# Kernel tuning notes

Hardware: AMD Instinct MI355X
Metric: run time of the kernel (lower is better)

## Reference

```python
import jax, jax.numpy as jnp
import numpy as np

DIM = 1024
HID = 256
MAXT = 2048
B = 4
T = 2048


def setup_inputs() -> dict:
    key = jax.random.key(0)
    ks = jax.random.split(key, 10)
    s_in = 1.0 / np.sqrt(DIM)   # keeps K ~ N(0,1) so exp(K) is stable
    s_h = 1.0 / np.sqrt(HID)
    # xavier-uniform bound for square wbias: sqrt(6/(T+T))
    wb_bound = float(np.sqrt(6.0 / (MAXT + MAXT)))
    return {
        "x": jax.random.normal(ks[0], (B, T, DIM), dtype=jnp.float32),
        "Wq": jax.random.normal(ks[1], (DIM, HID), dtype=jnp.float32) * s_in,
        "bq": jnp.zeros((HID,), dtype=jnp.float32),
        "Wk": jax.random.normal(ks[2], (DIM, HID), dtype=jnp.float32) * s_in,
        "bk": jnp.zeros((HID,), dtype=jnp.float32),
        "Wv": jax.random.normal(ks[3], (DIM, HID), dtype=jnp.float32) * s_in,
        "bv": jnp.zeros((HID,), dtype=jnp.float32),
        "Wp": jax.random.normal(ks[4], (HID, DIM), dtype=jnp.float32) * s_h,
        "bp": jnp.zeros((DIM,), dtype=jnp.float32),
        "wbias": jax.random.uniform(ks[5], (MAXT, MAXT), dtype=jnp.float32,
                                    minval=-wb_bound, maxval=wb_bound),
    }


def reference(x, Wq, bq, Wk, bk, Wv, bv, Wp, bp, wbias):
    Bn, Tn, _ = x.shape
    Q = x @ Wq + bq            # [B,T,H]
    K = x @ Wk + bk            # [B,T,H]
    V = x @ Wv + bv            # [B,T,H]
    ew = jnp.exp(wbias[:Tn, :Tn])          # [T,T]
    eK = jnp.exp(K)                         # [B,T,H]
    num = jnp.einsum('ts,bsh->bth', ew, eK * V)   # [B,T,H]
    den = jnp.einsum('ts,bsh->bth', ew, eK)       # [B,T,H]
    Yt = jax.nn.sigmoid(Q) * (num / den)          # [B,T,H]
    return Yt @ Wp + bp                            # [B,T,DIM]
```

## Files before the change

### kernel.cpp

```cpp
#include <hip/hip_runtime.h>
#include <hip/hip_bf16.h>


typedef __attribute__((ext_vector_type(8))) short bf16x8;
typedef __attribute__((ext_vector_type(4))) float f32x4;

static __device__ __forceinline__ unsigned short f2b(float f) {
  __hip_bfloat16 h = __float2bfloat16(f);
  return __builtin_bit_cast(unsigned short, h);
}

static __device__ __forceinline__ void gld16(const void* g, const void* l) {
  __builtin_amdgcn_global_load_lds((const __attribute__((address_space(1))) void*)g,
                                   (__attribute__((address_space(3))) void*)l, 16, 0, 0);
}

static __device__ __forceinline__ void core128(
    const unsigned short* __restrict__ A_blk,
    const unsigned short* __restrict__ Bt_blk,
    long sA, long sB, int nk, char* AsB, char* BsB, f32x4 acc[4][4],
    int tid, int wr, int wc, int fr, int fkb)
{
  const int srow = tid >> 2;
  const int sk   = (tid & 3) * 8;
  const unsigned short* ap0 = A_blk + (long)srow * sA + sk;
  const unsigned short* ap1 = ap0 + 64 * sA;
  const unsigned short* bp0 = Bt_blk + (long)srow * sB + sk;
  const unsigned short* bp1 = bp0 + 64 * sB;
  char* la0 = AsB + tid * 16;
  char* la1 = AsB + 4096 + tid * 16;
  char* lb0 = BsB + tid * 16;
  char* lb1 = BsB + 4096 + tid * 16;

  for (int kt = 0; kt < nk; ++kt) {
    gld16(ap0, la0);
    gld16(ap1, la1);
    gld16(bp0, lb0);
    gld16(bp1, lb1);
    ap0 += 32; ap1 += 32; bp0 += 32; bp1 += 32;
    asm volatile("s_waitcnt vmcnt(0)" ::: "memory");
    __syncthreads();

    bf16x8 av[4], bv[4];
#pragma unroll
    for (int m = 0; m < 4; ++m)
      av[m] = *(const bf16x8*)(AsB + (wr * 64 + m * 16 + fr) * 64 + fkb);
#pragma unroll
    for (int n = 0; n < 4; ++n)
      bv[n] = *(const bf16x8*)(BsB + (wc * 64 + n * 16 + fr) * 64 + fkb);
#pragma unroll
    for (int m = 0; m < 4; ++m)
#pragma unroll
      for (int n = 0; n < 4; ++n)
        acc[m][n] = __builtin_amdgcn_mfma_f32_16x16x32_bf16(av[m], bv[n], acc[m][n], 0, 0, 0);
    __syncthreads();
  }
}

__global__ __launch_bounds__(256) void gemm_bt(
    const unsigned short* __restrict__ A, const unsigned short* __restrict__ Bt,
    float* __restrict__ C, const float* __restrict__ bias,
    int M, int N, int K, int Ksub)
{
  __shared__ char AsB[8192];
  __shared__ char BsB[8192];
  const int tid = threadIdx.x, lane = tid & 63, wave = tid >> 6;
  const int wr = wave >> 1, wc = wave & 1;
  const int fr = lane & 15, fkb = (lane >> 4) * 16, q4 = (lane >> 4) * 4;
  const long bm = (long)blockIdx.y * 128;
  const long bn = (long)blockIdx.x * 128;
  const long k0 = (long)blockIdx.z * Ksub;

  f32x4 acc[4][4] = {};
  core128(A + bm * K + k0, Bt + bn * K + k0, K, K, Ksub >> 5,
          AsB, BsB, acc, tid, wr, wc, fr, fkb);

  float* Cz = C + (long)blockIdx.z * M * (long)N;
  const long crow0 = bm + wr * 64 + q4;
  const long ccol0 = bn + wc * 64 + fr;
#pragma unroll
  for (int n = 0; n < 4; ++n) {
    const long col = ccol0 + n * 16;
    const float bb = bias ? bias[col] : 0.f;
#pragma unroll
    for (int m = 0; m < 4; ++m)
#pragma unroll
      for (int r = 0; r < 4; ++r)
        Cz[(crow0 + m * 16 + r) * (long)N + col] = acc[m][n][r] + bb;
  }
}

__global__ __launch_bounds__(256) void gemm1_qkv(
    const unsigned short* __restrict__ xb, const unsigned short* __restrict__ WqkvT,
    const float* __restrict__ biascat,
    float* __restrict__ sgQ, unsigned short* __restrict__ B2T)
{
  __shared__ char AsB[8192];
  __shared__ char BsB[8192];
  const int tid = threadIdx.x, lane = tid & 63, wave = tid >> 6;
  const int wr = wave >> 1, wc = wave & 1;
  const int fr = lane & 15, fkb = (lane >> 4) * 16, q4 = (lane >> 4) * 4;
  const long bm = (long)blockIdx.y * 128;
  const long bn = (long)blockIdx.x * 128;
  const int  b  = (int)(bm >> 11);
  const int  tb = (int)(bm & 2047);

  f32x4 acc[4][4] = {};
  core128(xb + bm * 1024, WqkvT + bn * 1024, 1024, 1024, 32,
          AsB, BsB, acc, tid, wr, wc, fr, fkb);

  if (bn < 256) {
#pragma unroll
    for (int n = 0; n < 4; ++n) {
      const int col = (int)bn + wc * 64 + n * 16 + fr;
      const float bb = biascat[col];
#pragma unroll
      for (int m = 0; m < 4; ++m)
#pragma unroll
        for (int r = 0; r < 4; ++r) {
          long row = bm + wr * 64 + m * 16 + q4 + r;
          float v = acc[m][n][r] + bb;
          sgQ[row * 256 + col] = 1.f / (1.f + __expf(-v));
        }
    }
  } else {
#pragma unroll
    for (int n = 0; n < 4; ++n) {
      const int col = (int)bn + wc * 64 + n * 16 + fr;
      const int u   = col - 256;
      const float bb = biascat[col];
      const bool isK = (u & 1) == 0;
      const long rw = (long)b * 512 + u + (isK ? 1 : -1);
#pragma unroll
      for (int m = 0; m < 4; ++m) {
        float v[4], o[4];
#pragma unroll
        for (int r = 0; r < 4; ++r) v[r] = acc[m][n][r] + bb;
#pragma unroll
        for (int r = 0; r < 4; ++r) o[r] = __shfl_xor(v[r], 1);
        ushort4 pk;
        if (isK) {
          pk.x = f2b(__expf(v[0])); pk.y = f2b(__expf(v[1]));
          pk.z = f2b(__expf(v[2])); pk.w = f2b(__expf(v[3]));
        } else {
          pk.x = f2b(__expf(o[0]) * v[0]); pk.y = f2b(__expf(o[1]) * v[1]);
          pk.z = f2b(__expf(o[2]) * v[2]); pk.w = f2b(__expf(o[3]) * v[3]);
        }
        const int t0 = tb + wr * 64 + m * 16 + q4;
        *(ushort4*)(B2T + rw * 2048 + t0) = pk;
      }
    }
  }
}

__global__ void elt2_kernel(const float* __restrict__ C2, const float* __restrict__ sgQ,
                            unsigned short* __restrict__ Yt, int nslices) {
  int idx = blockIdx.x * 256 + threadIdx.x;
  int h = idx & 255, m = idx >> 8;
  int b = m >> 11, tt = m & 2047;
  long p2 = ((long)tt * 2048 + b * 512) >> 1;
  const float2* C22 = (const float2*)C2;
  float num = 0.f, den = 0.f;
  for (int z = 0; z < nslices; ++z) {
    float2 nd = C22[(long)z * 2097152 + p2 + h];
    num += nd.x; den += nd.y;
  }
  Yt[idx] = f2b(sgQ[idx] * num / den);
}

__global__ void prep_kernel(const float* __restrict__ x, const float* __restrict__ wbias,
                            const float* __restrict__ Wq, const float* __restrict__ Wk,
                            const float* __restrict__ Wv, const float* __restrict__ bq,
                            const float* __restrict__ bk, const float* __restrict__ bv,
                            const float* __restrict__ Wp,
                            unsigned short* __restrict__ xb, unsigned short* __restrict__ ewb,
                            unsigned short* __restrict__ WqkvT, unsigned short* __restrict__ WpT,
                            float* __restrict__ biascat) {
  const int bid = blockIdx.x;
  const int t = threadIdx.x;
  if (bid < 8192) {
    int i = bid * 256 + t;
    float4 v = ((const float4*)x)[i];
    ushort4 o; o.x = f2b(v.x); o.y = f2b(v.y); o.z = f2b(v.z); o.w = f2b(v.w);
    ((ushort4*)xb)[i] = o;
  } else if (bid < 12288) {
    int i = (bid - 8192) * 256 + t;
    float4 v = ((const float4*)wbias)[i];
    ushort4 o;
    o.x = f2b(__expf(v.x)); o.y = f2b(__expf(v.y));
    o.z = f2b(__expf(v.z)); o.w = f2b(__expf(v.w));
    ((ushort4*)ewb)[i] = o;
  } else {
    int idx = (bid - 12288) * 256 + t;
    if (idx < 768 * 1024) {
      int n = idx >> 10, k = idx & 1023;
      const float* W; int c;
      if (n < 256) { W = Wq; c = n; }
      else { int u = n - 256; c = u >> 1; W = (u & 1) ? Wv : Wk; }
      WqkvT[idx] = f2b(W[k * 256 + c]);
    }
    if (idx < 1024 * 256) {
      int d = idx >> 8, h = idx & 255;
      WpT[idx] = f2b(Wp[h * 1024 + d]);
    }
    if (idx < 768) {
      float v;
      if (idx < 256) v = bq[idx];
      else { int u = idx - 256; v = (u & 1) ? bv[u >> 1] : bk[u >> 1]; }
      biascat[idx] = v;
    }
  }
}

extern "C" void kernel_launch(void* const* d_in, const int* in_sizes, int n_in,
                              void* d_out, int out_size, void* d_ws, size_t ws_size,
                              hipStream_t stream) {
  const float* x     = (const float*)d_in[0];
  const float* Wq    = (const float*)d_in[1];
  const float* bq    = (const float*)d_in[2];
  const float* Wk    = (const float*)d_in[3];
  const float* bk    = (const float*)d_in[4];
  const float* Wv    = (const float*)d_in[5];
  const float* bv    = (const float*)d_in[6];
  const float* Wp    = (const float*)d_in[7];
  const float* bp    = (const float*)d_in[8];
  const float* wbias = (const float*)d_in[9];

  int nslices = 1;
  if (ws_size >= 4ull * 16777216 + 31461376) nslices = 4;
  else if (ws_size >= 2ull * 16777216 + 31461376) nslices = 2;

  char* ws = (char*)d_ws;
  const long base = (long)nslices * 16777216;
  unsigned short* xb      = (unsigned short*)(ws + 0);
  float*          C2      = (float*)(ws + 0);
  unsigned short* ewb     = (unsigned short*)(ws + base);
  unsigned short* WqkvT   = (unsigned short*)(ws + base + 8388608);
  unsigned short* WpT     = (unsigned short*)(ws + base + 9961472);
  float*          biascat = (float*)(ws + base + 10485760);
  float*          sgQ     = (float*)(ws + base + 10489856);
  unsigned short* B2T     = (unsigned short*)(ws + base + 18878464);
  unsigned short* Yt      = (unsigned short*)(ws + base + 27267072);
  float* out = (float*)d_out;

  prep_kernel<<<15360, 256, 0, stream>>>(x, wbias, Wq, Wk, Wv, bq, bk, bv, Wp,
                                         xb, ewb, WqkvT, WpT, biascat);
  gemm1_qkv<<<dim3(6, 64), 256, 0, stream>>>(xb, WqkvT, biascat, sgQ, B2T);
  gemm_bt<<<dim3(16, 16, nslices), 256, 0, stream>>>(ewb, B2T, C2, nullptr,
                                                     2048, 2048, 2048, 2048 / nslices);
  elt2_kernel<<<8192, 256, 0, stream>>>(C2, sgQ, Yt, nslices);
  gemm_bt<<<dim3(8, 64, 1), 256, 0, stream>>>(Yt, WpT, out, bp, 8192, 1024, 256, 256);
}
```

Before: 207.6 us.

## Drop split-K for the time-mixing GEMM and widen the K tile to 64

Removes the split-K path (up to 4 K slices) for the 2048x2048x2048 GEMM, so each block writes its full result directly. This cuts the extra partial-sum writes to the workspace and the reduction reads in the elementwise kernel. The shared GEMM core now stages a K depth of 64 per iteration instead of 32, which halves the number of barrier and wait rounds at the cost of doubled LDS per block. The big GEMM drops to 256 blocks, which may leave little latency hiding per CU. The workspace layout is also fixed at a fixed size instead of adapting to ws_size.

New measurement: 209.4 us. About the same (+0.9%).

```diff
diff --git a/kernel.cpp b/kernel.cpp
--- a/kernel.cpp
+++ b/kernel.cpp
@@ -15,67 +15,74 @@
                                    (__attribute__((address_space(3))) void*)l, 16, 0, 0);
 }
 
-static __device__ __forceinline__ void core128(
+static __device__ __forceinline__ void core128_bk64(
     const unsigned short* __restrict__ A_blk,
     const unsigned short* __restrict__ Bt_blk,
     long sA, long sB, int nk, char* AsB, char* BsB, f32x4 acc[4][4],
     int tid, int wr, int wc, int fr, int fkb)
 {
-  const int srow = tid >> 2;
-  const int sk   = (tid & 3) * 8;
+  const int srow = tid >> 3;
+  const int sk   = (tid & 7) * 8;
   const unsigned short* ap0 = A_blk + (long)srow * sA + sk;
-  const unsigned short* ap1 = ap0 + 64 * sA;
+  const unsigned short* ap1 = ap0 + 32 * sA;
+  const unsigned short* ap2 = ap0 + 64 * sA;
+  const unsigned short* ap3 = ap0 + 96 * sA;
   const unsigned short* bp0 = Bt_blk + (long)srow * sB + sk;
-  const unsigned short* bp1 = bp0 + 64 * sB;
-  char* la0 = AsB + tid * 16;
-  char* la1 = AsB + 4096 + tid * 16;
-  char* lb0 = BsB + tid * 16;
-  char* lb1 = BsB + 4096 + tid * 16;
+  const unsigned short* bp1 = bp0 + 32 * sB;
+  const unsigned short* bp2 = bp0 + 64 * sB;
+  const unsigned short* bp3 = bp0 + 96 * sB;
+  char* la = AsB + tid * 16;
+  char* lb = BsB + tid * 16;
 
   for (int kt = 0; kt < nk; ++kt) {
-    gld16(ap0, la0);
-    gld16(ap1, la1);
-    gld16(bp0, lb0);
-    gld16(bp1, lb1);
-    ap0 += 32; ap1 += 32; bp0 += 32; bp1 += 32;
+    gld16(ap0, la);
+    gld16(ap1, la + 4096);
+    gld16(ap2, la + 8192);
+    gld16(ap3, la + 12288);
+    gld16(bp0, lb);
+    gld16(bp1, lb + 4096);
+    gld16(bp2, lb + 8192);
+    gld16(bp3, lb + 12288);
+    ap0 += 64; ap1 += 64; ap2 += 64; ap3 += 64;
+    bp0 += 64; bp1 += 64; bp2 += 64; bp3 += 64;
     asm volatile("s_waitcnt vmcnt(0)" ::: "memory");
     __syncthreads();
 
-    bf16x8 av[4], bv[4];
-#pragma unroll
-    for (int m = 0; m < 4; ++m)
-      av[m] = *(const bf16x8*)(AsB + (wr * 64 + m * 16 + fr) * 64 + fkb);
-#pragma unroll
-    for (int n = 0; n < 4; ++n)
-      bv[n] = *(const bf16x8*)(BsB + (wc * 64 + n * 16 + fr) * 64 + fkb);
-#pragma unroll
-    for (int m = 0; m < 4; ++m)
+#pragma unroll
+    for (int kk = 0; kk < 2; ++kk) {
+      bf16x8 av[4], bv[4];
+#pragma unroll
+      for (int m = 0; m < 4; ++m)
+        av[m] = *(const bf16x8*)(AsB + (wr * 64 + m * 16 + fr) * 128 + kk * 64 + fkb);
 #pragma unroll
       for (int n = 0; n < 4; ++n)
-        acc[m][n] = __builtin_amdgcn_mfma_f32_16x16x32_bf16(av[m], bv[n], acc[m][n], 0, 0, 0);
+        bv[n] = *(const bf16x8*)(BsB + (wc * 64 + n * 16 + fr) * 128 + kk * 64 + fkb);
+#pragma unroll
+      for (int m = 0; m < 4; ++m)
+#pragma unroll
+        for (int n = 0; n < 4; ++n)
+          acc[m][n] = __builtin_amdgcn_mfma_f32_16x16x32_bf16(av[m], bv[n], acc[m][n], 0, 0, 0);
+    }
     __syncthreads();
   }
 }
 
 __global__ __launch_bounds__(256) void gemm_bt(
     const unsigned short* __restrict__ A, const unsigned short* __restrict__ Bt,
-    float* __restrict__ C, const float* __restrict__ bias,
-    int M, int N, int K, int Ksub)
+    float* __restrict__ C, const float* __restrict__ bias, int M, int N, int K)
 {
-  __shared__ char AsB[8192];
-  __shared__ char BsB[8192];
+  __shared__ char AsB[16384];
+  __shared__ char BsB[16384];
   const int tid = threadIdx.x, lane = tid & 63, wave = tid >> 6;
   const int wr = wave >> 1, wc = wave & 1;
   const int fr = lane & 15, fkb = (lane >> 4) * 16, q4 = (lane >> 4) * 4;
   const long bm = (long)blockIdx.y * 128;
   const long bn = (long)blockIdx.x * 128;
-  const long k0 = (long)blockIdx.z * Ksub;
 
   f32x4 acc[4][4] = {};
-  core128(A + bm * K + k0, Bt + bn * K + k0, K, K, Ksub >> 5,
-          AsB, BsB, acc, tid, wr, wc, fr, fkb);
-
-  float* Cz = C + (long)blockIdx.z * M * (long)N;
+  core128_bk64(A + bm * K, Bt + bn * K, K, K, K >> 6,
+               AsB, BsB, acc, tid, wr, wc, fr, fkb);
+
   const long crow0 = bm + wr * 64 + q4;
   const long ccol0 = bn + wc * 64 + fr;
 #pragma unroll
@@ -86,7 +93,7 @@
     for (int m = 0; m < 4; ++m)
 #pragma unroll
       for (int r = 0; r < 4; ++r)
-        Cz[(crow0 + m * 16 + r) * (long)N + col] = acc[m][n][r] + bb;
+        C[(crow0 + m * 16 + r) * (long)N + col] = acc[m][n][r] + bb;
   }
 }
 
@@ -95,8 +102,8 @@
     const float* __restrict__ biascat,
     float* __restrict__ sgQ, unsigned short* __restrict__ B2T)
 {
-  __shared__ char AsB[8192];
-  __shared__ char BsB[8192];
+  __shared__ char AsB[16384];
+  __shared__ char BsB[16384];
   const int tid = threadIdx.x, lane = tid & 63, wave = tid >> 6;
   const int wr = wave >> 1, wc = wave & 1;
   const int fr = lane & 15, fkb = (lane >> 4) * 16, q4 = (lane >> 4) * 4;
@@ -106,8 +113,8 @@
   const int  tb = (int)(bm & 2047);
 
   f32x4 acc[4][4] = {};
-  core128(xb + bm * 1024, WqkvT + bn * 1024, 1024, 1024, 32,
-          AsB, BsB, acc, tid, wr, wc, fr, fkb);
+  core128_bk64(xb + bm * 1024, WqkvT + bn * 1024, 1024, 1024, 16,
+               AsB, BsB, acc, tid, wr, wc, fr, fkb);
 
   if (bn < 256) {
 #pragma unroll
@@ -154,18 +161,13 @@
 }
 
 __global__ void elt2_kernel(const float* __restrict__ C2, const float* __restrict__ sgQ,
-                            unsigned short* __restrict__ Yt, int nslices) {
+                            unsigned short* __restrict__ Yt) {
   int idx = blockIdx.x * 256 + threadIdx.x;
   int h = idx & 255, m = idx >> 8;
   int b = m >> 11, tt = m & 2047;
   long p2 = ((long)tt * 2048 + b * 512) >> 1;
-  const float2* C22 = (const float2*)C2;
-  float num = 0.f, den = 0.f;
-  for (int z = 0; z < nslices; ++z) {
-    float2 nd = C22[(long)z * 2097152 + p2 + h];
-    num += nd.x; den += nd.y;
-  }
-  Yt[idx] = f2b(sgQ[idx] * num / den);
+  float2 nd = ((const float2*)C2)[p2 + h];
+  Yt[idx] = f2b(sgQ[idx] * nd.x / nd.y);
 }
 
 __global__ void prep_kernel(const float* __restrict__ x, const float* __restrict__ wbias,
@@ -226,28 +228,22 @@
   const float* bp    = (const float*)d_in[8];
   const float* wbias = (const float*)d_in[9];
 
-  int nslices = 1;
-  if (ws_size >= 4ull * 16777216 + 31461376) nslices = 4;
-  else if (ws_size >= 2ull * 16777216 + 31461376) nslices = 2;
-
   char* ws = (char*)d_ws;
-  const long base = (long)nslices * 16777216;
   unsigned short* xb      = (unsigned short*)(ws + 0);
-  float*          C2      = (float*)(ws + 0);
-  unsigned short* ewb     = (unsigned short*)(ws + base);
-  unsigned short* WqkvT   = (unsigned short*)(ws + base + 8388608);
-  unsigned short* WpT     = (unsigned short*)(ws + base + 9961472);
-  float*          biascat = (float*)(ws + base + 10485760);
-  float*          sgQ     = (float*)(ws + base + 10489856);
-  unsigned short* B2T     = (unsigned short*)(ws + base + 18878464);
-  unsigned short* Yt      = (unsigned short*)(ws + base + 27267072);
+  float*          C2      = (float*)(ws + 16777216);
+  unsigned short* ewb     = (unsigned short*)(ws + 33554432);
+  unsigned short* WqkvT   = (unsigned short*)(ws + 41943040);
+  unsigned short* WpT     = (unsigned short*)(ws + 43515904);
+  float*          biascat = (float*)(ws + 44040192);
+  float*          sgQ     = (float*)(ws + 44044288);
+  unsigned short* B2T     = (unsigned short*)(ws + 52432896);
+  unsigned short* Yt      = (unsigned short*)(ws + 60821504);
   float* out = (float*)d_out;
 
   prep_kernel<<<15360, 256, 0, stream>>>(x, wbias, Wq, Wk, Wv, bq, bk, bv, Wp,
                                          xb, ewb, WqkvT, WpT, biascat);
   gemm1_qkv<<<dim3(6, 64), 256, 0, stream>>>(xb, WqkvT, biascat, sgQ, B2T);
-  gemm_bt<<<dim3(16, 16, nslices), 256, 0, stream>>>(ewb, B2T, C2, nullptr,
-                                                     2048, 2048, 2048, 2048 / nslices);
-  elt2_kernel<<<8192, 256, 0, stream>>>(C2, sgQ, Yt, nslices);
-  gemm_bt<<<dim3(8, 64, 1), 256, 0, stream>>>(Yt, WpT, out, bp, 8192, 1024, 256, 256);
-}
+  gemm_bt<<<dim3(16, 16), 256, 0, stream>>>(ewb, B2T, C2, nullptr, 2048, 2048, 2048);
+  elt2_kernel<<<8192, 256, 0, stream>>>(C2, sgQ, Yt);
+  gemm_bt<<<dim3(8, 64), 256, 0, stream>>>(Yt, WpT, out, bp, 8192, 1024, 256);
+}
```

## Swizzle LDS GEMM tiles with K=64, narrow QKV tiles, stage B2T stores via LDS

Applied to the files above, without the earlier changes.

The GEMM core now loads K-tiles of 64 instead of 32 into an XOR-swizzled LDS layout, so each sync covers twice the MFMA work and bank conflicts on fragment reads drop. The QKV GEMM uses 128x64 tiles, doubling its grid. Its transposed exp(K)/exp(K)*V output is staged through swizzled LDS so global stores become coalesced 16-byte rows. The workspace layout also changes: C2 no longer aliases xb, and split-K is capped at 2 slices. The costs are higher LDS usage per block and possibly fewer split-K slices for the big GEMM.

Result: faster. 186.2 us (-10.3%).

```diff
diff --git a/kernel.cpp b/kernel.cpp
--- a/kernel.cpp
+++ b/kernel.cpp
@@ -15,44 +15,52 @@
                                    (__attribute__((address_space(3))) void*)l, 16, 0, 0);
 }
 
-static __device__ __forceinline__ void core128(
+template <int BN>
+static __device__ __forceinline__ void core_swz(
     const unsigned short* __restrict__ A_blk,
     const unsigned short* __restrict__ Bt_blk,
-    long sA, long sB, int nk, char* AsB, char* BsB, f32x4 acc[4][4],
-    int tid, int wr, int wc, int fr, int fkb)
+    long sA, long sB, int nk, char* AsB, char* BsB, f32x4 (&acc)[4][BN / 32],
+    int tid, int wr, int wc, int fr, int g)
 {
-  const int srow = tid >> 2;
-  const int sk   = (tid & 3) * 8;
-  const unsigned short* ap0 = A_blk + (long)srow * sA + sk;
-  const unsigned short* ap1 = ap0 + 64 * sA;
-  const unsigned short* bp0 = Bt_blk + (long)srow * sB + sk;
-  const unsigned short* bp1 = bp0 + 64 * sB;
-  char* la0 = AsB + tid * 16;
-  char* la1 = AsB + 4096 + tid * 16;
-  char* lb0 = BsB + tid * 16;
-  char* lb1 = BsB + 4096 + tid * 16;
+  const int srow = tid >> 3;
+  const int sslot = (tid & 7) ^ (srow & 7);
+  const unsigned short* ap = A_blk + (long)srow * sA + sslot * 8;
+  const unsigned short* bp = Bt_blk + (long)srow * sB + sslot * 8;
+  char* la = AsB + tid * 16;
+  char* lb = BsB + tid * 16;
+  const int xr = fr & 7;
 
   for (int kt = 0; kt < nk; ++kt) {
-    gld16(ap0, la0);
-    gld16(ap1, la1);
-    gld16(bp0, lb0);
-    gld16(bp1, lb1);
-    ap0 += 32; ap1 += 32; bp0 += 32; bp1 += 32;
+    gld16(ap,           la);
+    gld16(ap + 32 * sA, la + 4096);
+    gld16(ap + 64 * sA, la + 8192);
+    gld16(ap + 96 * sA, la + 12288);
+    gld16(bp,           lb);
+    gld16(bp + 32 * sB, lb + 4096);
+    if constexpr (BN == 128) {
+      gld16(bp + 64 * sB, lb + 8192);
+      gld16(bp + 96 * sB, lb + 12288);
+    }
+    ap += 64; bp += 64;
     asm volatile("s_waitcnt vmcnt(0)" ::: "memory");
     __syncthreads();
 
-    bf16x8 av[4], bv[4];
-#pragma unroll
-    for (int m = 0; m < 4; ++m)
-      av[m] = *(const bf16x8*)(AsB + (wr * 64 + m * 16 + fr) * 64 + fkb);
-#pragma unroll
-    for (int n = 0; n < 4; ++n)
-      bv[n] = *(const bf16x8*)(BsB + (wc * 64 + n * 16 + fr) * 64 + fkb);
-#pragma unroll
-    for (int m = 0; m < 4; ++m)
-#pragma unroll
-      for (int n = 0; n < 4; ++n)
-        acc[m][n] = __builtin_amdgcn_mfma_f32_16x16x32_bf16(av[m], bv[n], acc[m][n], 0, 0, 0);
+#pragma unroll
+    for (int kk = 0; kk < 2; ++kk) {
+      const int soff = ((kk * 4 + g) ^ xr) * 16;
+      bf16x8 av[4], bv[BN / 32];
+#pragma unroll
+      for (int m = 0; m < 4; ++m)
+        av[m] = *(const bf16x8*)(AsB + (wr * 64 + m * 16 + fr) * 128 + soff);
+#pragma unroll
+      for (int n = 0; n < BN / 32; ++n)
+        bv[n] = *(const bf16x8*)(BsB + (wc * (BN / 2) + n * 16 + fr) * 128 + soff);
+#pragma unroll
+      for (int m = 0; m < 4; ++m)
+#pragma unroll
+        for (int n = 0; n < BN / 32; ++n)
+          acc[m][n] = __builtin_amdgcn_mfma_f32_16x16x32_bf16(av[m], bv[n], acc[m][n], 0, 0, 0);
+    }
     __syncthreads();
   }
 }
@@ -62,18 +70,18 @@
     float* __restrict__ C, const float* __restrict__ bias,
     int M, int N, int K, int Ksub)
 {
-  __shared__ char AsB[8192];
-  __shared__ char BsB[8192];
+  __shared__ char AsB[16384];
+  __shared__ char BsB[16384];
   const int tid = threadIdx.x, lane = tid & 63, wave = tid >> 6;
   const int wr = wave >> 1, wc = wave & 1;
-  const int fr = lane & 15, fkb = (lane >> 4) * 16, q4 = (lane >> 4) * 4;
+  const int fr = lane & 15, g = lane >> 4, q4 = g * 4;
   const long bm = (long)blockIdx.y * 128;
   const long bn = (long)blockIdx.x * 128;
   const long k0 = (long)blockIdx.z * Ksub;
 
   f32x4 acc[4][4] = {};
-  core128(A + bm * K + k0, Bt + bn * K + k0, K, K, Ksub >> 5,
-          AsB, BsB, acc, tid, wr, wc, fr, fkb);
+  core_swz<128>(A + bm * K + k0, Bt + bn * K + k0, K, K, Ksub >> 6,
+                AsB, BsB, acc, tid, wr, wc, fr, g);
 
   float* Cz = C + (long)blockIdx.z * M * (long)N;
   const long crow0 = bm + wr * 64 + q4;
@@ -95,24 +103,24 @@
     const float* __restrict__ biascat,
     float* __restrict__ sgQ, unsigned short* __restrict__ B2T)
 {
-  __shared__ char AsB[8192];
+  __shared__ char AsB[16384];
   __shared__ char BsB[8192];
   const int tid = threadIdx.x, lane = tid & 63, wave = tid >> 6;
   const int wr = wave >> 1, wc = wave & 1;
-  const int fr = lane & 15, fkb = (lane >> 4) * 16, q4 = (lane >> 4) * 4;
+  const int fr = lane & 15, g = lane >> 4, q4 = g * 4;
   const long bm = (long)blockIdx.y * 128;
-  const long bn = (long)blockIdx.x * 128;
+  const long bn = (long)blockIdx.x * 64;
   const int  b  = (int)(bm >> 11);
   const int  tb = (int)(bm & 2047);
 
-  f32x4 acc[4][4] = {};
-  core128(xb + bm * 1024, WqkvT + bn * 1024, 1024, 1024, 32,
-          AsB, BsB, acc, tid, wr, wc, fr, fkb);
+  f32x4 acc[4][2] = {};
+  core_swz<64>(xb + bm * 1024, WqkvT + bn * 1024, 1024, 1024, 16,
+               AsB, BsB, acc, tid, wr, wc, fr, g);
 
   if (bn < 256) {
 #pragma unroll
-    for (int n = 0; n < 4; ++n) {
-      const int col = (int)bn + wc * 64 + n * 16 + fr;
+    for (int n = 0; n < 2; ++n) {
+      const int col = (int)bn + wc * 32 + n * 16 + fr;
       const float bb = biascat[col];
 #pragma unroll
       for (int m = 0; m < 4; ++m)
@@ -125,12 +133,12 @@
     }
   } else {
 #pragma unroll
-    for (int n = 0; n < 4; ++n) {
-      const int col = (int)bn + wc * 64 + n * 16 + fr;
-      const int u   = col - 256;
+    for (int n = 0; n < 2; ++n) {
+      const int col  = (int)bn + wc * 32 + n * 16 + fr;
+      const int u_in = wc * 32 + n * 16 + fr;
       const float bb = biascat[col];
-      const bool isK = (u & 1) == 0;
-      const long rw = (long)b * 512 + u + (isK ? 1 : -1);
+      const bool isK = (fr & 1) == 0;
+      const int u_tgt = u_in + (isK ? 1 : -1);
 #pragma unroll
       for (int m = 0; m < 4; ++m) {
         float v[4], o[4];
@@ -146,9 +154,21 @@
           pk.x = f2b(__expf(o[0]) * v[0]); pk.y = f2b(__expf(o[1]) * v[1]);
           pk.z = f2b(__expf(o[2]) * v[2]); pk.w = f2b(__expf(o[3]) * v[3]);
         }
-        const int t0 = tb + wr * 64 + m * 16 + q4;
-        *(ushort4*)(B2T + rw * 2048 + t0) = pk;
+        const int t_local = wr * 64 + m * 16 + q4;
+        const int slot16  = t_local >> 3;
+        const int addr = u_tgt * 256 + ((slot16 ^ (u_tgt & 15)) << 4)
+                       + ((t_local * 2) & 15);
+        *(ushort4*)(AsB + addr) = pk;
       }
+    }
+    __syncthreads();
+#pragma unroll
+    for (int i = 0; i < 4; ++i) {
+      int idx = tid + 256 * i;
+      int u = idx >> 4, s = idx & 15;
+      uint4 val = *(const uint4*)(AsB + u * 256 + ((s ^ (u & 15)) << 4));
+      long rw = (long)b * 512 + (bn - 256) + u;
+      *(uint4*)(B2T + rw * 2048 + tb + s * 8) = val;
     }
   }
 }
@@ -226,26 +246,24 @@
   const float* bp    = (const float*)d_in[8];
   const float* wbias = (const float*)d_in[9];
 
-  int nslices = 1;
-  if (ws_size >= 4ull * 16777216 + 31461376) nslices = 4;
-  else if (ws_size >= 2ull * 16777216 + 31461376) nslices = 2;
+  const int nslices = (ws_size >= 81803264ull) ? 2 : 1;
 
   char* ws = (char*)d_ws;
-  const long base = (long)nslices * 16777216;
+  const long rest0 = 16777216 + (long)nslices * 16777216;
   unsigned short* xb      = (unsigned short*)(ws + 0);
-  float*          C2      = (float*)(ws + 0);
-  unsigned short* ewb     = (unsigned short*)(ws + base);
-  unsigned short* WqkvT   = (unsigned short*)(ws + base + 8388608);
-  unsigned short* WpT     = (unsigned short*)(ws + base + 9961472);
-  float*          biascat = (float*)(ws + base + 10485760);
-  float*          sgQ     = (float*)(ws + base + 10489856);
-  unsigned short* B2T     = (unsigned short*)(ws + base + 18878464);
-  unsigned short* Yt      = (unsigned short*)(ws + base + 27267072);
+  float*          C2      = (float*)(ws + 16777216);
+  unsigned short* ewb     = (unsigned short*)(ws + rest0);
+  unsigned short* WqkvT   = (unsigned short*)(ws + rest0 + 8388608);
+  unsigned short* WpT     = (unsigned short*)(ws + rest0 + 9961472);
+  float*          biascat = (float*)(ws + rest0 + 10485760);
+  float*          sgQ     = (float*)(ws + rest0 + 10489856);
+  unsigned short* B2T     = (unsigned short*)(ws + rest0 + 18878464);
+  unsigned short* Yt      = (unsigned short*)(ws + rest0 + 27267072);
   float* out = (float*)d_out;
 
   prep_kernel<<<15360, 256, 0, stream>>>(x, wbias, Wq, Wk, Wv, bq, bk, bv, Wp,
                                          xb, ewb, WqkvT, WpT, biascat);
-  gemm1_qkv<<<dim3(6, 64), 256, 0, stream>>>(xb, WqkvT, biascat, sgQ, B2T);
+  gemm1_qkv<<<dim3(12, 64), 256, 0, stream>>>(xb, WqkvT, biascat, sgQ, B2T);
   gemm_bt<<<dim3(16, 16, nslices), 256, 0, stream>>>(ewb, B2T, C2, nullptr,
                                                      2048, 2048, 2048, 2048 / nslices);
   elt2_kernel<<<8192, 256, 0, stream>>>(C2, sgQ, Yt, nslices);
```
